# Performance work log

Measured on AMD Instinct MI355X. Metric: run time of the kernel, lower is better.

Reference implementation:

```python
import jax, jax.numpy as jnp
import numpy as np
import math
jax.config.update("jax_enable_x64", True)

# dims matching init_kwargs
BS, N_IND, N_STEP, ORDER = 32, 8, 100, 2
N_ORD = ORDER + 1            # number of derivative orders tracked (y, y', y'')
N_IV, N_IV_STEPS = 2, 1
NVAR = N_STEP * N_ORD        # qp variables per ODE (eps column is dropped: A[..., 1:])
DT = jnp.float64             # solver_dbl=True


def _static_parts():
    # initial-value constraint rows: u[t, j] = iv_rhs for t < n_iv_steps, j < n_iv
    iv_rows = N_IV_STEPS * N_IV
    Iv = np.zeros((iv_rows, NVAR))
    r = 0
    for t in range(N_IV_STEPS):
        for j in range(N_IV):
            Iv[r, t * N_ORD + j] = 1.0
            r += 1
    # Taylor expansion tables: fact[i, j] = 1/(j-i)! for j>=i else 0; expn[i,j] = j-i
    i_idx = np.arange(ORDER)[:, None]
    j_idx = np.arange(N_ORD)[None, :]
    dmask = j_idx >= i_idx
    d = np.where(dmask, j_idx - i_idx, 0)
    fact = np.where(dmask, 1.0 / np.array([[math.factorial(v) for v in row] for row in d]), 0.0)
    sign = np.where(dmask, (-1.0) ** d, 0.0)
    Imat = np.eye(ORDER, N_ORD)
    return (jnp.asarray(Iv, DT), jnp.asarray(fact, DT), jnp.asarray(d, DT),
            jnp.asarray(sign, DT), jnp.asarray(Imat, DT))


def _solve(coeffs, rhs, iv_rhs, steps):
    # coeffs: (B, n_step, n_ord), rhs: (B, n_step), iv_rhs: (B, iv_rows), steps: (B, n_step-1)
    B = coeffs.shape[0]
    T1 = N_STEP - 1
    R = 2 * ORDER + 1  # fwd Taylor rows (ORDER) + bwd Taylor rows (ORDER) + central row (1)
    Iv, fact, expn, sign, Imat = _static_parts()

    # equation constraints: block-diagonal in step: sum_j coeffs[b,t,j] * u[t,j] = rhs[b,t]
    eye = jnp.eye(N_STEP, dtype=DT)
    Eq = jnp.einsum('ts,bsj->btsj', eye, coeffs).reshape(B, N_STEP, NVAR)
    IvB = jnp.broadcast_to(Iv[None], (B,) + Iv.shape)

    # smoothness constraints per interval t -> t+1 with step h = steps[b,t]
    h = steps[:, :, None, None]                  # (B, T1, 1, 1)
    hp = h ** expn                               # h^(j-i)
    fwd_t = fact * hp                            # fwd Taylor: sum_j h^(j-i)/(j-i)! u[t,j] - u[t+1,i] = 0
    bwd_t1 = fact * sign * hp                    # bwd Taylor: sum_j (-h)^(j-i)/(j-i)! u[t+1,j] - u[t,i] = 0
    ImB = jnp.broadcast_to(Imat, fwd_t.shape)
    hh = steps[:, :, None]                       # (B, T1, 1)
    e_m1 = jnp.zeros((N_ORD,), DT).at[ORDER - 1].set(1.0)
    e_o = jnp.zeros((N_ORD,), DT).at[ORDER].set(1.0)
    # central (trapezoid) rule on highest derivative:
    # u[t+1,ord-1] - u[t,ord-1] - h/2 (u[t,ord] + u[t+1,ord]) = 0
    ct = -e_m1 - 0.5 * hh * e_o                  # (B, T1, n_ord) coeffs on block t
    ct1 = e_m1 - 0.5 * hh * e_o                  # coeffs on block t+1
    Dt = jnp.concatenate([fwd_t, -ImB, ct[:, :, None, :]], axis=2)    # (B,T1,R,n_ord)
    Dt1 = jnp.concatenate([-ImB, bwd_t1, ct1[:, :, None, :]], axis=2)

    Dfull = jnp.zeros((B, T1, R, N_STEP, N_ORD), DT)
    t = jnp.arange(T1)
    Dfull = Dfull.at[:, t, :, t, :].set(jnp.moveaxis(Dt, 1, 0))
    Dfull = Dfull.at[:, t, :, t + 1, :].set(jnp.moveaxis(Dt1, 1, 0))
    D = Dfull.reshape(B, T1 * R, NVAR)

    A = jnp.concatenate([Eq, IvB, D], axis=1)    # dense AG (eps column dropped)
    beta = jnp.concatenate([rhs, iv_rhs, jnp.zeros((B, T1 * R), DT)], axis=1)

    AtA = jnp.einsum('bmi,bmj->bij', A, A)
    Atb = jnp.einsum('bmi,bm->bi', A, beta)
    L = jnp.linalg.cholesky(AtA)
    x = jax.scipy.linalg.cho_solve((L, True), Atb[..., None])[..., 0]
    return x


def setup_inputs() -> dict:
    key = jax.random.key(0)
    k1, k2, k3, k4 = jax.random.split(key, 4)
    coeffs = jax.random.normal(k1, (BS, N_IND, N_STEP, N_ORD), dtype=jnp.float32)
    rhs = jax.random.normal(k2, (BS, N_IND, N_STEP), dtype=jnp.float32)
    iv_rhs = jax.random.normal(k3, (BS, N_IND, N_IV_STEPS * N_IV), dtype=jnp.float32)
    # positive step sizes around the module's step_size=0.1
    steps = 0.05 + 0.1 * jax.random.uniform(k4, (BS, N_IND, N_STEP - 1), dtype=jnp.float32)
    return {"coeffs": coeffs, "rhs": rhs, "iv_rhs": iv_rhs, "steps": steps}


def reference(coeffs, rhs, iv_rhs, steps):
    B = BS * N_IND
    c = coeffs.reshape(B, N_STEP, N_ORD).astype(DT)   # n_dim = 1 folded in
    r = rhs.reshape(B, N_STEP).astype(DT)
    iv = iv_rhs.reshape(B, N_IV_STEPS * N_IV).astype(DT)
    st = steps.reshape(B, N_STEP - 1).astype(DT)
    x = _solve(c, r, iv, st)
    u = x.reshape(BS, N_IND, N_STEP, N_ORD)
    u0, u1, u2 = u[..., 0], u[..., 1], u[..., 2]
    eps = jnp.zeros((B,), DT)
    return (u0, u1, u2, eps, st[:, :, None])
```

## Files before the change

kernel.cpp:

```cpp
#include <hip/hip_runtime.h>
#include <math.h>

#define NPROB 256
#define NSTEP 100
#define T1    99

__global__ __launch_bounds__(128) void ode_cr_kernel(
    const float* __restrict__ coeffs,
    const float* __restrict__ rhs,
    const float* __restrict__ iv_rhs,
    const float* __restrict__ steps,
    float* __restrict__ out)
{
    const int b   = blockIdx.x;
    const int tid = threadIdx.x;

    __shared__ double A[NSTEP][6];
    __shared__ double C[NSTEP][9];
    __shared__ double bb[NSTEP][3];
    __shared__ double P[NSTEP][9];
    __shared__ double Q[NSTEP][9];
    __shared__ double z[NSTEP][3];
    __shared__ double X[NSTEP][3];

    const float* cb = coeffs + b * NSTEP * 3;
    const float* rb = rhs    + b * NSTEP;
    const float* sb = steps  + b * T1;

    if (tid < NSTEP) {
        const int t = tid;
        const double c0 = (double)cb[t * 3 + 0];
        const double c1 = (double)cb[t * 3 + 1];
        const double c2 = (double)cb[t * 3 + 2];
        const double r  = (double)rb[t];

        double a00 = c0 * c0, a01 = c0 * c1, a02 = c0 * c2;
        double a11 = c1 * c1, a12 = c1 * c2, a22 = c2 * c2;
        double b0 = c0 * r, b1 = c1 * r, b2 = c2 * r;

        if (t == 0) {
            a00 += 1.0; a11 += 1.0;
            b0 += (double)iv_rhs[b * 2 + 0];
            b1 += (double)iv_rhs[b * 2 + 1];
        }
        if (t < T1) {
            const double h = (double)sb[t], h2 = h * h;
            a00 += 2.0;
            a01 += h;
            a02 += 0.5 * h2;
            a11 += h2 + 3.0;
            a12 += 0.5 * h2 * h + 1.5 * h;
            a22 += 0.25 * h2 * h2 + 1.25 * h2;
        }
        if (t > 0) {
            const double hm = (double)sb[t - 1], hm2 = hm * hm;
            a00 += 2.0;
            a01 -= hm;
            a02 += 0.5 * hm2;
            a11 += hm2 + 3.0;
            a12 -= 0.5 * hm2 * hm + 1.5 * hm;
            a22 += 0.25 * hm2 * hm2 + 1.25 * hm2;

            C[t][0] = -2.0;       C[t][1] = -hm;       C[t][2] = -0.5 * hm2;
            C[t][3] =  hm;        C[t][4] = -3.0;      C[t][5] = -1.5 * hm;
            C[t][6] = -0.5 * hm2; C[t][7] =  1.5 * hm; C[t][8] =  0.25 * hm2;
        }
        A[t][0] = a00; A[t][1] = a01; A[t][2] = a02;
        A[t][3] = a11; A[t][4] = a12; A[t][5] = a22;
        bb[t][0] = b0; bb[t][1] = b1; bb[t][2] = b2;
    }
    __syncthreads();

    int ncount[8];
    int n = NSTEP, stride = 1, nlev = 0;
    while (n > 1) {
        ncount[nlev] = n;

        int j = 2 * tid + 1;
        if (j < n) {
            const int t = j * stride;
            const double a00 = A[t][0], a01 = A[t][1], a02 = A[t][2];
            const double a11 = A[t][3], a12 = A[t][4], a22 = A[t][5];
            const double l00 = sqrt(a00), i0 = 1.0 / l00;
            const double l10 = a01 * i0, l20 = a02 * i0;
            const double l11 = sqrt(a11 - l10 * l10), i1 = 1.0 / l11;
            const double l21 = (a12 - l20 * l10) * i1;
            const double l22 = sqrt(a22 - l20 * l20 - l21 * l21), i2 = 1.0 / l22;

#define SOLVE3(in0, in1, in2, o0, o1, o2)                                   \
            {                                                               \
                const double f0 = (in0) * i0;                               \
                const double f1 = ((in1) - l10 * f0) * i1;                  \
                const double f2 = ((in2) - l20 * f0 - l21 * f1) * i2;       \
                o2 = f2 * i2;                                               \
                o1 = (f1 - l21 * o2) * i1;                                  \
                o0 = (f0 - l10 * o1 - l20 * o2) * i0;                       \
            }

            for (int k = 0; k < 3; ++k) {
                double o0, o1, o2;
                SOLVE3(C[t][k], C[t][3 + k], C[t][6 + k], o0, o1, o2);
                P[t][k] = o0; P[t][3 + k] = o1; P[t][6 + k] = o2;
            }
            if (j + 1 < n) {
                const int tr = t + stride;
                for (int k = 0; k < 3; ++k) {
                    double o0, o1, o2;
                    SOLVE3(C[tr][3 * k], C[tr][3 * k + 1], C[tr][3 * k + 2], o0, o1, o2);
                    Q[t][k] = o0; Q[t][3 + k] = o1; Q[t][6 + k] = o2;
                }
            }
            {
                double o0, o1, o2;
                SOLVE3(bb[t][0], bb[t][1], bb[t][2], o0, o1, o2);
                z[t][0] = o0; z[t][1] = o1; z[t][2] = o2;
            }
#undef SOLVE3
        }
        __syncthreads();

        j = 2 * tid;
        if (j < n) {
            const int t = j * stride;
            double a00 = A[t][0], a01 = A[t][1], a02 = A[t][2];
            double a11 = A[t][3], a12 = A[t][4], a22 = A[t][5];
            double b0 = bb[t][0], b1 = bb[t][1], b2 = bb[t][2];
            double nc[9];
            const bool hasL = (j > 0);
            if (hasL) {
                const int ti = t - stride;
                double Ct[9];
                for (int k = 0; k < 9; ++k) Ct[k] = C[t][k];
                const double* Qi = Q[ti];
                a00 -= Ct[0] * Qi[0] + Ct[1] * Qi[3] + Ct[2] * Qi[6];
                a01 -= Ct[0] * Qi[1] + Ct[1] * Qi[4] + Ct[2] * Qi[7];
                a02 -= Ct[0] * Qi[2] + Ct[1] * Qi[5] + Ct[2] * Qi[8];
                a11 -= Ct[3] * Qi[1] + Ct[4] * Qi[4] + Ct[5] * Qi[7];
                a12 -= Ct[3] * Qi[2] + Ct[4] * Qi[5] + Ct[5] * Qi[8];
                a22 -= Ct[6] * Qi[2] + Ct[7] * Qi[5] + Ct[8] * Qi[8];
                const double* Pi = P[ti];
                for (int r0 = 0; r0 < 3; ++r0)
                    for (int c0 = 0; c0 < 3; ++c0)
                        nc[3 * r0 + c0] = -(Ct[3 * r0] * Pi[c0] +
                                            Ct[3 * r0 + 1] * Pi[3 + c0] +
                                            Ct[3 * r0 + 2] * Pi[6 + c0]);
                const double* zi = z[ti];
                b0 -= Ct[0] * zi[0] + Ct[1] * zi[1] + Ct[2] * zi[2];
                b1 -= Ct[3] * zi[0] + Ct[4] * zi[1] + Ct[5] * zi[2];
                b2 -= Ct[6] * zi[0] + Ct[7] * zi[1] + Ct[8] * zi[2];
            }
            if (j + 1 < n) {
                const int ti = t + stride;
                double Cr[9];
                for (int k = 0; k < 9; ++k) Cr[k] = C[ti][k];
                const double* Pi = P[ti];
                a00 -= Cr[0] * Pi[0] + Cr[3] * Pi[3] + Cr[6] * Pi[6];
                a01 -= Cr[0] * Pi[1] + Cr[3] * Pi[4] + Cr[6] * Pi[7];
                a02 -= Cr[0] * Pi[2] + Cr[3] * Pi[5] + Cr[6] * Pi[8];
                a11 -= Cr[1] * Pi[1] + Cr[4] * Pi[4] + Cr[7] * Pi[7];
                a12 -= Cr[1] * Pi[2] + Cr[4] * Pi[5] + Cr[7] * Pi[8];
                a22 -= Cr[2] * Pi[2] + Cr[5] * Pi[5] + Cr[8] * Pi[8];
                const double* zi = z[ti];
                b0 -= Cr[0] * zi[0] + Cr[3] * zi[1] + Cr[6] * zi[2];
                b1 -= Cr[1] * zi[0] + Cr[4] * zi[1] + Cr[7] * zi[2];
                b2 -= Cr[2] * zi[0] + Cr[5] * zi[1] + Cr[8] * zi[2];
            }
            A[t][0] = a00; A[t][1] = a01; A[t][2] = a02;
            A[t][3] = a11; A[t][4] = a12; A[t][5] = a22;
            bb[t][0] = b0; bb[t][1] = b1; bb[t][2] = b2;
            if (hasL)
                for (int k = 0; k < 9; ++k) C[t][k] = nc[k];
        }
        __syncthreads();

        n = (n + 1) / 2;
        stride *= 2;
        ++nlev;
    }

    if (tid == 0) {
        const double a00 = A[0][0], a01 = A[0][1], a02 = A[0][2];
        const double a11 = A[0][3], a12 = A[0][4], a22 = A[0][5];
        const double l00 = sqrt(a00), i0 = 1.0 / l00;
        const double l10 = a01 * i0, l20 = a02 * i0;
        const double l11 = sqrt(a11 - l10 * l10), i1 = 1.0 / l11;
        const double l21 = (a12 - l20 * l10) * i1;
        const double l22 = sqrt(a22 - l20 * l20 - l21 * l21), i2 = 1.0 / l22;
        const double f0 = bb[0][0] * i0;
        const double f1 = (bb[0][1] - l10 * f0) * i1;
        const double f2 = (bb[0][2] - l20 * f0 - l21 * f1) * i2;
        const double x2 = f2 * i2;
        const double x1 = (f1 - l21 * x2) * i1;
        const double x0 = (f0 - l10 * x1 - l20 * x2) * i0;
        X[0][0] = x0; X[0][1] = x1; X[0][2] = x2;
    }
    __syncthreads();

    for (int lev = nlev - 1; lev >= 0; --lev) {
        stride >>= 1;
        const int nl = ncount[lev];
        const int j = 2 * tid + 1;
        if (j < nl) {
            const int t = j * stride;
            const double* xl = X[t - stride];
            double v0 = z[t][0], v1 = z[t][1], v2 = z[t][2];
            v0 -= P[t][0] * xl[0] + P[t][1] * xl[1] + P[t][2] * xl[2];
            v1 -= P[t][3] * xl[0] + P[t][4] * xl[1] + P[t][5] * xl[2];
            v2 -= P[t][6] * xl[0] + P[t][7] * xl[1] + P[t][8] * xl[2];
            if (j + 1 < nl) {
                const double* xr = X[t + stride];
                v0 -= Q[t][0] * xr[0] + Q[t][1] * xr[1] + Q[t][2] * xr[2];
                v1 -= Q[t][3] * xr[0] + Q[t][4] * xr[1] + Q[t][5] * xr[2];
                v2 -= Q[t][6] * xr[0] + Q[t][7] * xr[1] + Q[t][8] * xr[2];
            }
            X[t][0] = v0; X[t][1] = v1; X[t][2] = v2;
        }
        __syncthreads();
    }

    if (tid < NSTEP) {
        const int t = tid;
        out[            b * NSTEP + t] = (float)X[t][0];
        out[25600 +     b * NSTEP + t] = (float)X[t][1];
        out[51200 +     b * NSTEP + t] = (float)X[t][2];
        if (t < T1)
            out[77056 + b * T1 + t] = sb[t];
    }
    if (tid == 0)
        out[76800 + b] = 0.0f;
}

extern "C" void kernel_launch(void* const* d_in, const int* in_sizes, int n_in,
                              void* d_out, int out_size, void* d_ws, size_t ws_size,
                              hipStream_t stream) {
    const float* coeffs = (const float*)d_in[0];
    const float* rhs    = (const float*)d_in[1];
    const float* iv_rhs = (const float*)d_in[2];
    const float* steps  = (const float*)d_in[3];
    float* out = (float*)d_out;

    ode_cr_kernel<<<dim3(NPROB), dim3(128), 0, stream>>>(
        coeffs, rhs, iv_rhs, steps, out);
}
```

Before: 70.56 us.

## Use explicit 3x3 inverse, single-wavefront blocks, and fully unrolled reduction levels

Replaces the per-block Cholesky factorization (three fp64 sqrt and three reciprocals) with an adjugate-based symmetric 3x3 inverse, so each block needs one fp64 divide followed by matrix-vector products. The block shrinks to 64 threads, one wavefront, and the setup and output loops become strided. The cyclic-reduction level counts are hardcoded so both level loops can be fully unrolled. The explicit inverse can be less numerically stable than Cholesky on ill-conditioned blocks.

```diff
diff --git a/kernel.cpp b/kernel.cpp
--- a/kernel.cpp
+++ b/kernel.cpp
@@ -1,11 +1,10 @@
 #include <hip/hip_runtime.h>
-#include <math.h>
 
 #define NPROB 256
 #define NSTEP 100
 #define T1    99
 
-__global__ __launch_bounds__(128) void ode_cr_kernel(
+__global__ __launch_bounds__(64) void ode_cr_kernel(
     const float* __restrict__ coeffs,
     const float* __restrict__ rhs,
     const float* __restrict__ iv_rhs,
@@ -27,8 +26,7 @@
     const float* rb = rhs    + b * NSTEP;
     const float* sb = steps  + b * T1;
 
-    if (tid < NSTEP) {
-        const int t = tid;
+    for (int t = tid; t < NSTEP; t += 64) {
         const double c0 = (double)cb[t * 3 + 0];
         const double c1 = (double)cb[t * 3 + 1];
         const double c2 = (double)cb[t * 3 + 2];
@@ -71,51 +69,51 @@
     }
     __syncthreads();
 
-    int ncount[8];
-    int n = NSTEP, stride = 1, nlev = 0;
-    while (n > 1) {
-        ncount[nlev] = n;
+    const int NC[7] = {100, 50, 25, 13, 7, 4, 2};
+
+#pragma unroll
+    for (int lev = 0; lev < 7; ++lev) {
+        const int n = NC[lev];
+        const int stride = 1 << lev;
 
         int j = 2 * tid + 1;
         if (j < n) {
             const int t = j * stride;
             const double a00 = A[t][0], a01 = A[t][1], a02 = A[t][2];
             const double a11 = A[t][3], a12 = A[t][4], a22 = A[t][5];
-            const double l00 = sqrt(a00), i0 = 1.0 / l00;
-            const double l10 = a01 * i0, l20 = a02 * i0;
-            const double l11 = sqrt(a11 - l10 * l10), i1 = 1.0 / l11;
-            const double l21 = (a12 - l20 * l10) * i1;
-            const double l22 = sqrt(a22 - l20 * l20 - l21 * l21), i2 = 1.0 / l22;
-
-#define SOLVE3(in0, in1, in2, o0, o1, o2)                                   \
-            {                                                               \
-                const double f0 = (in0) * i0;                               \
-                const double f1 = ((in1) - l10 * f0) * i1;                  \
-                const double f2 = ((in2) - l20 * f0 - l21 * f1) * i2;       \
-                o2 = f2 * i2;                                               \
-                o1 = (f1 - l21 * o2) * i1;                                  \
-                o0 = (f0 - l10 * o1 - l20 * o2) * i0;                       \
-            }
-
+            const double k00 = a11 * a22 - a12 * a12;
+            const double k01 = a02 * a12 - a01 * a22;
+            const double k02 = a01 * a12 - a02 * a11;
+            const double det = a00 * k00 + a01 * k01 + a02 * k02;
+            const double id  = 1.0 / det;
+            const double g00 = k00 * id;
+            const double g01 = k01 * id;
+            const double g02 = k02 * id;
+            const double g11 = (a00 * a22 - a02 * a02) * id;
+            const double g12 = (a02 * a01 - a00 * a12) * id;
+            const double g22 = (a00 * a11 - a01 * a01) * id;
+
+#pragma unroll
             for (int k = 0; k < 3; ++k) {
-                double o0, o1, o2;
-                SOLVE3(C[t][k], C[t][3 + k], C[t][6 + k], o0, o1, o2);
-                P[t][k] = o0; P[t][3 + k] = o1; P[t][6 + k] = o2;
+                const double c0k = C[t][k], c1k = C[t][3 + k], c2k = C[t][6 + k];
+                P[t][k]     = g00 * c0k + g01 * c1k + g02 * c2k;
+                P[t][3 + k] = g01 * c0k + g11 * c1k + g12 * c2k;
+                P[t][6 + k] = g02 * c0k + g12 * c1k + g22 * c2k;
             }
             if (j + 1 < n) {
                 const int tr = t + stride;
+#pragma unroll
                 for (int k = 0; k < 3; ++k) {
-                    double o0, o1, o2;
-                    SOLVE3(C[tr][3 * k], C[tr][3 * k + 1], C[tr][3 * k + 2], o0, o1, o2);
-                    Q[t][k] = o0; Q[t][3 + k] = o1; Q[t][6 + k] = o2;
+                    const double cr0 = C[tr][3 * k], cr1 = C[tr][3 * k + 1], cr2 = C[tr][3 * k + 2];
+                    Q[t][k]     = g00 * cr0 + g01 * cr1 + g02 * cr2;
+                    Q[t][3 + k] = g01 * cr0 + g11 * cr1 + g12 * cr2;
+                    Q[t][6 + k] = g02 * cr0 + g12 * cr1 + g22 * cr2;
                 }
             }
-            {
-                double o0, o1, o2;
-                SOLVE3(bb[t][0], bb[t][1], bb[t][2], o0, o1, o2);
-                z[t][0] = o0; z[t][1] = o1; z[t][2] = o2;
-            }
-#undef SOLVE3
+            const double b0 = bb[t][0], b1 = bb[t][1], b2 = bb[t][2];
+            z[t][0] = g00 * b0 + g01 * b1 + g02 * b2;
+            z[t][1] = g01 * b0 + g11 * b1 + g12 * b2;
+            z[t][2] = g02 * b0 + g12 * b1 + g22 * b2;
         }
         __syncthreads();
 
@@ -130,6 +128,7 @@
             if (hasL) {
                 const int ti = t - stride;
                 double Ct[9];
+#pragma unroll
                 for (int k = 0; k < 9; ++k) Ct[k] = C[t][k];
                 const double* Qi = Q[ti];
                 a00 -= Ct[0] * Qi[0] + Ct[1] * Qi[3] + Ct[2] * Qi[6];
@@ -139,7 +138,9 @@
                 a12 -= Ct[3] * Qi[2] + Ct[4] * Qi[5] + Ct[5] * Qi[8];
                 a22 -= Ct[6] * Qi[2] + Ct[7] * Qi[5] + Ct[8] * Qi[8];
                 const double* Pi = P[ti];
+#pragma unroll
                 for (int r0 = 0; r0 < 3; ++r0)
+#pragma unroll
                     for (int c0 = 0; c0 < 3; ++c0)
                         nc[3 * r0 + c0] = -(Ct[3 * r0] * Pi[c0] +
                                             Ct[3 * r0 + 1] * Pi[3 + c0] +
@@ -152,6 +153,7 @@
             if (j + 1 < n) {
                 const int ti = t + stride;
                 double Cr[9];
+#pragma unroll
                 for (int k = 0; k < 9; ++k) Cr[k] = C[ti][k];
                 const double* Pi = P[ti];
                 a00 -= Cr[0] * Pi[0] + Cr[3] * Pi[3] + Cr[6] * Pi[6];
@@ -169,45 +171,46 @@
             A[t][3] = a11; A[t][4] = a12; A[t][5] = a22;
             bb[t][0] = b0; bb[t][1] = b1; bb[t][2] = b2;
             if (hasL)
+#pragma unroll
                 for (int k = 0; k < 9; ++k) C[t][k] = nc[k];
         }
         __syncthreads();
-
-        n = (n + 1) / 2;
-        stride *= 2;
-        ++nlev;
     }
 
     if (tid == 0) {
         const double a00 = A[0][0], a01 = A[0][1], a02 = A[0][2];
         const double a11 = A[0][3], a12 = A[0][4], a22 = A[0][5];
-        const double l00 = sqrt(a00), i0 = 1.0 / l00;
-        const double l10 = a01 * i0, l20 = a02 * i0;
-        const double l11 = sqrt(a11 - l10 * l10), i1 = 1.0 / l11;
-        const double l21 = (a12 - l20 * l10) * i1;
-        const double l22 = sqrt(a22 - l20 * l20 - l21 * l21), i2 = 1.0 / l22;
-        const double f0 = bb[0][0] * i0;
-        const double f1 = (bb[0][1] - l10 * f0) * i1;
-        const double f2 = (bb[0][2] - l20 * f0 - l21 * f1) * i2;
-        const double x2 = f2 * i2;
-        const double x1 = (f1 - l21 * x2) * i1;
-        const double x0 = (f0 - l10 * x1 - l20 * x2) * i0;
-        X[0][0] = x0; X[0][1] = x1; X[0][2] = x2;
+        const double k00 = a11 * a22 - a12 * a12;
+        const double k01 = a02 * a12 - a01 * a22;
+        const double k02 = a01 * a12 - a02 * a11;
+        const double det = a00 * k00 + a01 * k01 + a02 * k02;
+        const double id  = 1.0 / det;
+        const double g00 = k00 * id;
+        const double g01 = k01 * id;
+        const double g02 = k02 * id;
+        const double g11 = (a00 * a22 - a02 * a02) * id;
+        const double g12 = (a02 * a01 - a00 * a12) * id;
+        const double g22 = (a00 * a11 - a01 * a01) * id;
+        const double b0 = bb[0][0], b1 = bb[0][1], b2 = bb[0][2];
+        X[0][0] = g00 * b0 + g01 * b1 + g02 * b2;
+        X[0][1] = g01 * b0 + g11 * b1 + g12 * b2;
+        X[0][2] = g02 * b0 + g12 * b1 + g22 * b2;
     }
     __syncthreads();
 
-    for (int lev = nlev - 1; lev >= 0; --lev) {
-        stride >>= 1;
-        const int nl = ncount[lev];
+#pragma unroll
+    for (int lev = 6; lev >= 0; --lev) {
+        const int n = NC[lev];
+        const int stride = 1 << lev;
         const int j = 2 * tid + 1;
-        if (j < nl) {
+        if (j < n) {
             const int t = j * stride;
             const double* xl = X[t - stride];
             double v0 = z[t][0], v1 = z[t][1], v2 = z[t][2];
             v0 -= P[t][0] * xl[0] + P[t][1] * xl[1] + P[t][2] * xl[2];
             v1 -= P[t][3] * xl[0] + P[t][4] * xl[1] + P[t][5] * xl[2];
             v2 -= P[t][6] * xl[0] + P[t][7] * xl[1] + P[t][8] * xl[2];
-            if (j + 1 < nl) {
+            if (j + 1 < n) {
                 const double* xr = X[t + stride];
                 v0 -= Q[t][0] * xr[0] + Q[t][1] * xr[1] + Q[t][2] * xr[2];
                 v1 -= Q[t][3] * xr[0] + Q[t][4] * xr[1] + Q[t][5] * xr[2];
@@ -218,8 +221,7 @@
         __syncthreads();
     }
 
-    if (tid < NSTEP) {
-        const int t = tid;
+    for (int t = tid; t < NSTEP; t += 64) {
         out[            b * NSTEP + t] = (float)X[t][0];
         out[25600 +     b * NSTEP + t] = (float)X[t][1];
         out[51200 +     b * NSTEP + t] = (float)X[t][2];
@@ -239,6 +241,6 @@
     const float* steps  = (const float*)d_in[3];
     float* out = (float*)d_out;
 
-    ode_cr_kernel<<<dim3(NPROB), dim3(128), 0, stream>>>(
+    ode_cr_kernel<<<dim3(NPROB), dim3(64), 0, stream>>>(
         coeffs, rhs, iv_rhs, steps, out);
 }
```

Result: no change. 70.42 us (-0.2%).
